# Kernel optimization log

Hardware: AMD Instinct MI355X
Metric: run time of the kernel (lower is better)

## Reference

```python
import jax, jax.numpy as jnp
import numpy as np

D_MODEL = 1024
N_HEAD = 16
AGENT_NUM = 256


def setup_inputs() -> dict:
    key = jax.random.key(0)
    ks = jax.random.split(key, 11)
    B, S, D = 4, 2048, D_MODEL
    s = 1.0 / np.sqrt(D)
    return {
        "q": jax.random.normal(ks[0], (B, S, D), jnp.float32),
        "k": jax.random.normal(ks[1], (B, S, D), jnp.float32),
        "v": jax.random.normal(ks[2], (B, S, D), jnp.float32),
        "Wq": jax.random.normal(ks[3], (D, D), jnp.float32) * s,
        "bq": jnp.zeros((D,), jnp.float32),
        "Wk": jax.random.normal(ks[4], (D, D), jnp.float32) * s,
        "bk": jnp.zeros((D,), jnp.float32),
        "Wv": jax.random.normal(ks[5], (D, D), jnp.float32) * s,
        "bv": jnp.zeros((D,), jnp.float32),
        "Wo": jax.random.normal(ks[6], (D, D), jnp.float32) * s,
        "bo": jnp.zeros((D,), jnp.float32),
    }


def _split_heads(x, n_head):
    B, S, D = x.shape
    return x.reshape(B, S, n_head, D // n_head).transpose(0, 2, 1, 3)  # [B,H,S,d]


def reference(q, k, v, Wq, bq, Wk, bk, Wv, bv, Wo, bo):
    B, S, D = q.shape
    H, A = N_HEAD, AGENT_NUM
    d = D // H
    scale = 1.0 / jnp.sqrt(jnp.asarray(d, q.dtype))

    # QKV linear projections (torch Linear: x @ W.T + b)
    qh = _split_heads(q @ Wq.T + bq, H)  # [B,H,S,d]
    kh = _split_heads(k @ Wk.T + bk, H)
    vh = _split_heads(v @ Wv.T + bv, H)

    # Agent tokens: average-pool queries along sequence down to A tokens
    agent = qh.reshape(B, H, A, S // A, d).mean(axis=3)  # [B,H,A,d]

    # Stage 1: agents aggregate from keys/values (softmax over S)
    agent_attn = jax.nn.softmax(
        jnp.einsum("bhad,bhsd->bhas", agent, kh) * scale, axis=-1)  # [B,H,A,S]
    agent_v = jnp.einsum("bhas,bhsd->bhad", agent_attn, vh)  # [B,H,A,d]

    # Stage 2: queries attend to agent tokens (softmax over A)
    q_attn = jax.nn.softmax(
        jnp.einsum("bhsd,bhad->bhsa", qh, agent) * scale, axis=-1)  # [B,H,S,A]
    out_h = jnp.einsum("bhsa,bhad->bhsd", q_attn, agent_v)  # [B,H,S,d]

    # concat heads + output projection
    out = out_h.transpose(0, 2, 1, 3).reshape(B, S, D)
    out = out @ Wo.T + bo
    return out, q_attn
```

## Files before the change

### kernel.cpp

```cpp
#include <hip/hip_runtime.h>

constexpr int Bsz = 4, Ssz = 2048, Dsz = 1024, Hn = 16, dh = 64, An = 256;

typedef __attribute__((ext_vector_type(8))) short bf16x8;
typedef __attribute__((ext_vector_type(4))) float f32x4;

__device__ __forceinline__ unsigned short f2bf_rn(float f) {
    unsigned int u = __float_as_uint(f);
    return (unsigned short)((u + 0x7FFFu + ((u >> 16) & 1u)) >> 16);
}
__device__ __forceinline__ float bf2f(unsigned short h) {
    return __uint_as_float(((unsigned int)h) << 16);
}
__device__ __forceinline__ void bf_split(float f, unsigned short& hi, unsigned short& lo) {
    hi = f2bf_rn(f);
    lo = f2bf_rn(f - bf2f(hi));
}
__device__ __forceinline__ void gload16(const unsigned short* g, unsigned short* l) {
    __builtin_amdgcn_global_load_lds(
        (const __attribute__((address_space(1))) unsigned int*)g,
        (__attribute__((address_space(3))) unsigned int*)l, 16, 0, 0);
}
__device__ __forceinline__ bf16x8 gfrag(const unsigned short* g) {
    return *reinterpret_cast<const bf16x8*>(g);
}
__device__ __forceinline__ void make8(float4 a, float4 b, bf16x8& hi8, bf16x8& lo8) {
    float v[8] = {a.x, a.y, a.z, a.w, b.x, b.y, b.z, b.w};
    #pragma unroll
    for (int i = 0; i < 8; ++i) {
        unsigned short h, l;
        bf_split(v[i], h, l);
        hi8[i] = (short)h; lo8[i] = (short)l;
    }
}


template<int LOGC, int NISS>
__device__ __forceinline__ void stage_tile(const unsigned short* __restrict__ g, long rowStride,
                                           unsigned short* lbase, int t) {
    const int wid = t >> 6;
    #pragma unroll
    for (int i = 0; i < NISS; ++i) {
        int slot = i * 256 + t;
        int r = slot >> LOGC;
        int c = slot & ((1 << LOGC) - 1);
        int cs = (c ^ (r & 7)) & ((1 << LOGC) - 1);
        gload16(g + (long)r * rowStride + cs * 8, lbase + (i * 256 + wid * 64) * 8);
    }
}
template<int ROWLEN>
__device__ __forceinline__ bf16x8 fragR(const unsigned short* buf, int row, int ks, int lane) {
    int c = ks * 4 + (lane >> 4);
    int cs = (c ^ (row & 7)) & (ROWLEN / 8 - 1);
    return *reinterpret_cast<const bf16x8*>(buf + row * ROWLEN + cs * 8);
}

__global__ __launch_bounds__(256)
void split_kernel(const float* __restrict__ x, unsigned short* __restrict__ hi,
                  unsigned short* __restrict__ lo, int n4)
{
    int i = blockIdx.x * 256 + threadIdx.x;
    if (i >= n4) return;
    float4 v = reinterpret_cast<const float4*>(x)[i];
    ushort4 h, l;
    bf_split(v.x, h.x, l.x);
    bf_split(v.y, h.y, l.y);
    bf_split(v.z, h.z, l.z);
    bf_split(v.w, h.w, l.w);
    reinterpret_cast<ushort4*>(hi)[i] = h;
    reinterpret_cast<ushort4*>(lo)[i] = l;
}

#define MT 128
#define BKm 32

__device__ __forceinline__ bf16x8 lds_frag(const unsigned short* buf, int baseRow, int lane) {
    int row = baseRow + (lane & 15);
    int c = lane >> 4;
    int idx = row * 32 + ((c ^ ((row >> 1) & 3)) << 3);
    return *reinterpret_cast<const bf16x8*>(buf + idx);
}

template<int OMODE>
__global__ __launch_bounds__(256, 2)
void gemm_nt_mfma3(const unsigned short* __restrict__ Ahi, const unsigned short* __restrict__ Alo,
                   const unsigned short* __restrict__ Bhi, const unsigned short* __restrict__ Blo,
                   const float* __restrict__ bias, float* __restrict__ Cf,
                   unsigned short* __restrict__ Chi, unsigned short* __restrict__ Clo,
                   int K, int N)
{
    __shared__ unsigned short lds[4 * 4096];
    const int t = threadIdx.x;
    const int lane = t & 63, wid = t >> 6;
    const int wr = wid >> 1, wc = wid & 1;
    const int m0 = blockIdx.y * MT, n0 = blockIdx.x * MT;

    const int srow0 = t >> 2;
    const int x4 = t & 3;
    const int ldsBase0 = (wid * 64) * 8;
    const int ldsBase1 = (256 + wid * 64) * 8;

    f32x4 acc[4][4];
    #pragma unroll
    for (int i = 0; i < 4; ++i)
        #pragma unroll
        for (int j = 0; j < 4; ++j)
            acc[i][j] = f32x4{0.f, 0.f, 0.f, 0.f};

    const unsigned short* gA[2] = {Ahi, Alo};
    const unsigned short* gB[2] = {Bhi, Blo};

    for (int k0 = 0; k0 < K; k0 += BKm) {
        #pragma unroll
        for (int hb = 0; hb < 2; ++hb) {
            {
                const unsigned short* G = gA[hb];
                int r0 = srow0, r1 = srow0 + 64;
                int c0 = x4 ^ ((r0 >> 1) & 3);
                int c1 = x4 ^ ((r1 >> 1) & 3);
                gload16(G + (size_t)(m0 + r0) * K + k0 + c0 * 8, lds + hb * 4096 + ldsBase0);
                gload16(G + (size_t)(m0 + r1) * K + k0 + c1 * 8, lds + hb * 4096 + ldsBase1);
            }
            {
                const unsigned short* G = gB[hb];
                int r0 = srow0, r1 = srow0 + 64;
                int c0 = x4 ^ ((r0 >> 1) & 3);
                int c1 = x4 ^ ((r1 >> 1) & 3);
                gload16(G + (size_t)(n0 + r0) * K + k0 + c0 * 8, lds + (2 + hb) * 4096 + ldsBase0);
                gload16(G + (size_t)(n0 + r1) * K + k0 + c1 * 8, lds + (2 + hb) * 4096 + ldsBase1);
            }
        }
        __syncthreads();

        bf16x8 ah[4], al[4], bh[4], bl[4];
        #pragma unroll
        for (int mi = 0; mi < 4; ++mi) {
            ah[mi] = lds_frag(lds + 0 * 4096, wr * 64 + mi * 16, lane);
            al[mi] = lds_frag(lds + 1 * 4096, wr * 64 + mi * 16, lane);
        }
        #pragma unroll
        for (int ni = 0; ni < 4; ++ni) {
            bh[ni] = lds_frag(lds + 2 * 4096, wc * 64 + ni * 16, lane);
            bl[ni] = lds_frag(lds + 3 * 4096, wc * 64 + ni * 16, lane);
        }
        #pragma unroll
        for (int mi = 0; mi < 4; ++mi)
            #pragma unroll
            for (int ni = 0; ni < 4; ++ni) {
                acc[mi][ni] = __builtin_amdgcn_mfma_f32_16x16x32_bf16(ah[mi], bh[ni], acc[mi][ni], 0, 0, 0);
                acc[mi][ni] = __builtin_amdgcn_mfma_f32_16x16x32_bf16(ah[mi], bl[ni], acc[mi][ni], 0, 0, 0);
                acc[mi][ni] = __builtin_amdgcn_mfma_f32_16x16x32_bf16(al[mi], bh[ni], acc[mi][ni], 0, 0, 0);
            }
        __syncthreads();
    }

    #pragma unroll
    for (int mi = 0; mi < 4; ++mi) {
        #pragma unroll
        for (int ni = 0; ni < 4; ++ni) {
            const int n = n0 + wc * 64 + ni * 16 + (lane & 15);
            const float bval = bias[n];
            #pragma unroll
            for (int j = 0; j < 4; ++j) {
                const int m = m0 + wr * 64 + mi * 16 + ((lane >> 4) << 2) + j;
                float val = acc[mi][ni][j] + bval;
                if constexpr (OMODE == 0) {
                    Cf[(size_t)m * N + n] = val;
                } else {
                    const int b = m >> 11, s = m & (Ssz - 1);
                    const int h = n >> 6, c = n & (dh - 1);
                    size_t idx;
                    if constexpr (OMODE == 1)
                        idx = (((size_t)(b * Hn + h)) * Ssz + s) * dh + c;
                    else if constexpr (OMODE == 2)
                        idx = (((size_t)(b * Hn + h)) * dh + c) * Ssz + s;
                    else
                        idx = (size_t)(b * Hn + h) * 131072
                            + (((s >> 4) * 2 + (c >> 5)) << 9)
                            + (((c >> 3) & 3) << 7) + ((s & 15) << 3) + (c & 7);
                    unsigned short hi, lo;
                    bf_split(val, hi, lo);
                    Chi[idx] = hi; Clo[idx] = lo;
                }
            }
        }
    }
}

__global__ __launch_bounds__(256)
void pool_agent(const unsigned short* __restrict__ qh_hi, const unsigned short* __restrict__ qh_lo,
                unsigned short* __restrict__ ag_hi, unsigned short* __restrict__ ag_lo)
{
    const int idx = blockIdx.x * 256 + threadIdx.x;
    const int c = idx & (dh - 1);
    const int a = (idx >> 6) & (An - 1);
    const int bh = idx >> 14;
    const size_t base = (size_t)bh * 131072
        + (((a >> 1) * 2 + (c >> 5)) << 9) + (((c >> 3) & 3) << 7)
        + ((8 * (a & 1)) << 3) + (c & 7);
    float s = 0.f;
    #pragma unroll
    for (int j = 0; j < 8; ++j)
        s += bf2f(qh_hi[base + j * 8]) + bf2f(qh_lo[base + j * 8]);
    s *= 0.125f;
    unsigned short hi, lo;
    bf_split(s, hi, lo);
    const size_t oidx = (size_t)bh * 16384
        + (((a >> 4) * 2 + (c >> 5)) << 9) + (((c >> 3) & 3) << 7)
        + ((a & 15) << 3) + (c & 7);
    ag_hi[oidx] = hi; ag_lo[oidx] = lo;
}

__global__ __launch_bounds__(256, 3)
void flash1(const unsigned short* __restrict__ ag_hi, const unsigned short* __restrict__ ag_lo,
            const unsigned short* __restrict__ kh_hi, const unsigned short* __restrict__ kh_lo,
            const unsigned short* __restrict__ vt_hi_g, const unsigned short* __restrict__ vt_lo_g,
            unsigned short* __restrict__ avt_hi, unsigned short* __restrict__ avt_lo)
{
    __shared__ unsigned short lds[24576];
    unsigned short* kth = lds;
    unsigned short* ktl = lds + 4096;
    unsigned short* vth = lds + 8192;
    unsigned short* vtl = lds + 12288;
    const int t = threadIdx.x;
    const int lane = t & 63, w = t >> 6;
    const int al15 = lane & 15, hi4 = lane >> 4;
    unsigned short* pwh = lds + 16384 + w * 2048;
    unsigned short* pwl = pwh + 1024;

    const int bh = blockIdx.y;
    const int a0 = blockIdx.x * 64;

    bf16x8 bqh[2], bql[2];
    {
        const size_t abase = (size_t)bh * 16384 + (size_t)((a0 >> 4) + w) * 1024;
        #pragma unroll
        for (int ks = 0; ks < 2; ++ks) {
            bqh[ks] = gfrag(ag_hi + abase + ks * 512 + lane * 8);
            bql[ks] = gfrag(ag_lo + abase + ks * 512 + lane * 8);
        }
    }

    f32x4 O[4];
    #pragma unroll
    for (int i = 0; i < 4; ++i) O[i] = f32x4{0.f, 0.f, 0.f, 0.f};
    float m_run = -INFINITY, l_run = 0.f;

    for (int s0 = 0; s0 < Ssz; s0 += 64) {
        stage_tile<3, 2>(kh_hi + ((size_t)bh * Ssz + s0) * dh, dh, kth, t);
        stage_tile<3, 2>(kh_lo + ((size_t)bh * Ssz + s0) * dh, dh, ktl, t);
        stage_tile<3, 2>(vt_hi_g + (size_t)bh * dh * Ssz + s0, Ssz, vth, t);
        stage_tile<3, 2>(vt_lo_g + (size_t)bh * dh * Ssz + s0, Ssz, vtl, t);
        __syncthreads();

        f32x4 sc[4];
        #pragma unroll
        for (int si = 0; si < 4; ++si) sc[si] = f32x4{0.f, 0.f, 0.f, 0.f};
        #pragma unroll
        for (int si = 0; si < 4; ++si)
            #pragma unroll
            for (int ks = 0; ks < 2; ++ks) {
                bf16x8 ah = fragR<64>(kth, si * 16 + al15, ks, lane);
                bf16x8 al = fragR<64>(ktl, si * 16 + al15, ks, lane);
                sc[si] = __builtin_amdgcn_mfma_f32_16x16x32_bf16(ah, bqh[ks], sc[si], 0, 0, 0);
                sc[si] = __builtin_amdgcn_mfma_f32_16x16x32_bf16(ah, bql[ks], sc[si], 0, 0, 0);
                sc[si] = __builtin_amdgcn_mfma_f32_16x16x32_bf16(al, bqh[ks], sc[si], 0, 0, 0);
            }

        float tmax = -INFINITY;
        #pragma unroll
        for (int si = 0; si < 4; ++si)
            #pragma unroll
            for (int j = 0; j < 4; ++j) {
                sc[si][j] *= 0.125f;
                tmax = fmaxf(tmax, sc[si][j]);
            }
        tmax = fmaxf(tmax, __shfl_xor(tmax, 16));
        tmax = fmaxf(tmax, __shfl_xor(tmax, 32));
        float newm = fmaxf(m_run, tmax);
        float fac = __expf(m_run - newm);
        float tsum = 0.f;
        #pragma unroll
        for (int si = 0; si < 4; ++si)
            #pragma unroll
            for (int j = 0; j < 4; ++j) {
                float p = __expf(sc[si][j] - newm);
                sc[si][j] = p;
                tsum += p;
            }
        tsum += __shfl_xor(tsum, 16);
        tsum += __shfl_xor(tsum, 32);
        l_run = l_run * fac + tsum;
        m_run = newm;

        #pragma unroll
        for (int si = 0; si < 4; ++si) {
            ushort4 h4, l4;
            bf_split(sc[si][0], h4.x, l4.x);
            bf_split(sc[si][1], h4.y, l4.y);
            bf_split(sc[si][2], h4.z, l4.z);
            bf_split(sc[si][3], h4.w, l4.w);
            int baseS = si * 16 + (hi4 << 2);
            int addr = al15 * 64 + (baseS ^ ((al15 & 7) << 3));
            *reinterpret_cast<ushort4*>(pwh + addr) = h4;
            *reinterpret_cast<ushort4*>(pwl + addr) = l4;
        }

        float fj[4];
        #pragma unroll
        for (int j = 0; j < 4; ++j) fj[j] = __shfl(fac, (hi4 << 2) + j);
        #pragma unroll
        for (int di = 0; di < 4; ++di)
            #pragma unroll
            for (int j = 0; j < 4; ++j) O[di][j] *= fj[j];

        #pragma unroll
        for (int ks = 0; ks < 2; ++ks) {
            bf16x8 pah = fragR<64>(pwh, al15, ks, lane);
            bf16x8 pal = fragR<64>(pwl, al15, ks, lane);
            #pragma unroll
            for (int di = 0; di < 4; ++di) {
                bf16x8 vh = fragR<64>(vth, di * 16 + al15, ks, lane);
                bf16x8 vl = fragR<64>(vtl, di * 16 + al15, ks, lane);
                O[di] = __builtin_amdgcn_mfma_f32_16x16x32_bf16(pah, vh, O[di], 0, 0, 0);
                O[di] = __builtin_amdgcn_mfma_f32_16x16x32_bf16(pah, vl, O[di], 0, 0, 0);
                O[di] = __builtin_amdgcn_mfma_f32_16x16x32_bf16(pal, vh, O[di], 0, 0, 0);
            }
        }
        __syncthreads();
    }

    float lj[4];
    #pragma unroll
    for (int j = 0; j < 4; ++j) lj[j] = __shfl(l_run, (hi4 << 2) + j);
    #pragma unroll
    for (int di = 0; di < 4; ++di) {
        ushort4 h4, l4;
        #pragma unroll
        for (int j = 0; j < 4; ++j) {
            float val = O[di][j] / lj[j];
            unsigned short hi, lo;
            bf_split(val, hi, lo);
            ((unsigned short*)&h4)[j] = hi;
            ((unsigned short*)&l4)[j] = lo;
        }
        const size_t oidx = (size_t)bh * 16384
            + (size_t)(di * 8 + (a0 >> 5) + (w >> 1)) * 512
            + (size_t)((2 * w + (hi4 >> 1)) & 3) * 128
            + al15 * 8 + (hi4 & 1) * 4;
        *reinterpret_cast<ushort4*>(avt_hi + oidx) = h4;
        *reinterpret_cast<ushort4*>(avt_lo + oidx) = l4;
    }
}

__global__ __launch_bounds__(256, 2)
void flash2(const unsigned short* __restrict__ qh_hi, const unsigned short* __restrict__ qh_lo,
            const unsigned short* __restrict__ ag_hi, const unsigned short* __restrict__ ag_lo,
            const unsigned short* __restrict__ avt_hi, const unsigned short* __restrict__ avt_lo,
            float* __restrict__ q_attn,
            unsigned short* __restrict__ xo_hi, unsigned short* __restrict__ xo_lo)
{
    __shared__ float plds[4][4096];

    const int t = threadIdx.x, lane = t & 63, w = t >> 6;
    const int al15 = lane & 15, hi4 = lane >> 4;
    const int bh = blockIdx.y;
    const int s0 = blockIdx.x * 64;
    float* P = plds[w];

    bf16x8 bqh[2], bql[2];
    {
        const size_t qbase = (size_t)bh * 131072 + (size_t)((s0 >> 4) + w) * 1024;
        #pragma unroll
        for (int ks = 0; ks < 2; ++ks) {
            bqh[ks] = gfrag(qh_hi + qbase + ks * 512 + lane * 8);
            bql[ks] = gfrag(qh_lo + qbase + ks * 512 + lane * 8);
        }
    }

    const unsigned short* agh = ag_hi + (size_t)bh * 16384;
    const unsigned short* agl = ag_lo + (size_t)bh * 16384;
    f32x4 acc[16];
    #pragma unroll
    for (int ai = 0; ai < 16; ++ai) acc[ai] = f32x4{0.f, 0.f, 0.f, 0.f};
    #pragma unroll
    for (int ai = 0; ai < 16; ++ai)
        #pragma unroll
        for (int ks = 0; ks < 2; ++ks) {
            bf16x8 ah = gfrag(agh + (ai * 2 + ks) * 512 + lane * 8);
            bf16x8 al = gfrag(agl + (ai * 2 + ks) * 512 + lane * 8);
            acc[ai] = __builtin_amdgcn_mfma_f32_16x16x32_bf16(ah, bqh[ks], acc[ai], 0, 0, 0);
            acc[ai] = __builtin_amdgcn_mfma_f32_16x16x32_bf16(ah, bql[ks], acc[ai], 0, 0, 0);
            acc[ai] = __builtin_amdgcn_mfma_f32_16x16x32_bf16(al, bqh[ks], acc[ai], 0, 0, 0);
        }

    float mx = -INFINITY;
    #pragma unroll
    for (int ai = 0; ai < 16; ++ai)
        #pragma unroll
        for (int j = 0; j < 4; ++j) {
            acc[ai][j] *= 0.125f;
            mx = fmaxf(mx, acc[ai][j]);
        }
    mx = fmaxf(mx, __shfl_xor(mx, 16));
    mx = fmaxf(mx, __shfl_xor(mx, 32));
    float sum = 0.f;
    #pragma unroll
    for (int ai = 0; ai < 16; ++ai)
        #pragma unroll
        for (int j = 0; j < 4; ++j) {
            float p = __expf(acc[ai][j] - mx);
            acc[ai][j] = p;
            sum += p;
        }
    sum += __shfl_xor(sum, 16);
    sum += __shfl_xor(sum, 32);
    const float inv = 1.0f / sum;

    #pragma unroll
    for (int ai = 0; ai < 16; ++ai) {
        float4 o;
        o.x = acc[ai][0] * inv; o.y = acc[ai][1] * inv;
        o.z = acc[ai][2] * inv; o.w = acc[ai][3] * inv;
        int pos4 = (ai * 4 + hi4) ^ (al15 & 7);
        *reinterpret_cast<float4*>(P + al15 * 256 + pos4 * 4) = o;
    }

    {
        float* qbase = q_attn + ((size_t)bh * Ssz + s0 + w * 16) * An;
        #pragma unroll
        for (int r = 0; r < 16; ++r) {
            float4 f = *reinterpret_cast<const float4*>(P + r * 256 + ((lane ^ (r & 7)) * 4));
            *reinterpret_cast<float4*>(qbase + r * An + lane * 4) = f;
        }
    }

    const unsigned short* avh_b = avt_hi + (size_t)bh * 16384;
    const unsigned short* avl_b = avt_lo + (size_t)bh * 16384;
    f32x4 O[4];
    #pragma unroll
    for (int i = 0; i < 4; ++i) O[i] = f32x4{0.f, 0.f, 0.f, 0.f};
    #pragma unroll
    for (int ks = 0; ks < 8; ++ks) {
        int p4 = ks * 8 + hi4 * 2;
        float4 fa = *reinterpret_cast<const float4*>(P + al15 * 256 + ((p4 ^ (al15 & 7)) * 4));
        float4 fb = *reinterpret_cast<const float4*>(P + al15 * 256 + (((p4 + 1) ^ (al15 & 7)) * 4));
        bf16x8 pah, pal;
        make8(fa, fb, pah, pal);
        #pragma unroll
        for (int di = 0; di < 4; ++di) {
            bf16x8 avh = gfrag(avh_b + (di * 8 + ks) * 512 + lane * 8);
            bf16x8 avl = gfrag(avl_b + (di * 8 + ks) * 512 + lane * 8);
            O[di] = __builtin_amdgcn_mfma_f32_16x16x32_bf16(pah, avh, O[di], 0, 0, 0);
            O[di] = __builtin_amdgcn_mfma_f32_16x16x32_bf16(pah, avl, O[di], 0, 0, 0);
            O[di] = __builtin_amdgcn_mfma_f32_16x16x32_bf16(pal, avh, O[di], 0, 0, 0);
        }
    }

    const int b = bh >> 4, h = bh & (Hn - 1);
    #pragma unroll
    for (int di = 0; di < 4; ++di)
        #pragma unroll
        for (int j = 0; j < 4; ++j) {
            float val = O[di][j];
            int sG = s0 + w * 16 + (hi4 << 2) + j;
            int dfull = h * dh + di * 16 + al15;
            size_t idx = ((size_t)b * Ssz + sG) * Dsz + dfull;
            unsigned short hi, lo;
            bf_split(val, hi, lo);
            xo_hi[idx] = hi; xo_lo[idx] = lo;
        }
}

extern "C" void kernel_launch(void* const* d_in, const int* in_sizes, int n_in,
                              void* d_out, int out_size, void* d_ws, size_t ws_size,
                              hipStream_t stream)
{
    const float* q  = (const float*)d_in[0];
    const float* k  = (const float*)d_in[1];
    const float* v  = (const float*)d_in[2];
    const float* Wq = (const float*)d_in[3];
    const float* bq = (const float*)d_in[4];
    const float* Wk = (const float*)d_in[5];
    const float* bk = (const float*)d_in[6];
    const float* Wv = (const float*)d_in[7];
    const float* bv = (const float*)d_in[8];
    const float* Wo = (const float*)d_in[9];
    const float* bo = (const float*)d_in[10];

    constexpr size_t BSD = (size_t)Bsz * Ssz * Dsz;
    constexpr size_t DD  = (size_t)Dsz * Dsz;
    constexpr size_t AGD = (size_t)Bsz * Hn * An * dh;

    float* out    = (float*)d_out;
    float* q_attn = out + BSD;

    unsigned short* u = (unsigned short*)d_ws;
    unsigned short* x_hi   = u;
    unsigned short* x_lo   = x_hi + BSD;
    unsigned short* qh_hi  = x_lo + BSD;
    unsigned short* qh_lo  = qh_hi + BSD;
    unsigned short* kh_hi  = qh_lo + BSD;
    unsigned short* kh_lo  = kh_hi + BSD;
    unsigned short* vt_hi  = kh_lo + BSD;
    unsigned short* vt_lo  = vt_hi + BSD;
    unsigned short* w_hi   = vt_lo + BSD;
    unsigned short* w_lo   = w_hi + DD;
    unsigned short* ag_hi  = w_lo + DD;
    unsigned short* ag_lo  = ag_hi + AGD;
    unsigned short* avt_hi = ag_lo + AGD;
    unsigned short* avt_lo = avt_hi + AGD;

    const int M = Bsz * Ssz;
    dim3 gmfma(Dsz / MT, M / MT, 1);

    split_kernel<<<BSD / 1024, 256, 0, stream>>>(q, x_hi, x_lo, BSD / 4);
    split_kernel<<<DD / 1024, 256, 0, stream>>>(Wq, w_hi, w_lo, DD / 4);
    gemm_nt_mfma3<3><<<gmfma, 256, 0, stream>>>(x_hi, x_lo, w_hi, w_lo, bq, nullptr, qh_hi, qh_lo, Dsz, Dsz);
    split_kernel<<<BSD / 1024, 256, 0, stream>>>(k, x_hi, x_lo, BSD / 4);
    split_kernel<<<DD / 1024, 256, 0, stream>>>(Wk, w_hi, w_lo, DD / 4);
    gemm_nt_mfma3<1><<<gmfma, 256, 0, stream>>>(x_hi, x_lo, w_hi, w_lo, bk, nullptr, kh_hi, kh_lo, Dsz, Dsz);
    split_kernel<<<BSD / 1024, 256, 0, stream>>>(v, x_hi, x_lo, BSD / 4);
    split_kernel<<<DD / 1024, 256, 0, stream>>>(Wv, w_hi, w_lo, DD / 4);
    gemm_nt_mfma3<2><<<gmfma, 256, 0, stream>>>(x_hi, x_lo, w_hi, w_lo, bv, nullptr, vt_hi, vt_lo, Dsz, Dsz);

    pool_agent<<<AGD / 256, 256, 0, stream>>>(qh_hi, qh_lo, ag_hi, ag_lo);

    flash1<<<dim3(An / 64, Bsz * Hn), 256, 0, stream>>>(
        ag_hi, ag_lo, kh_hi, kh_lo, vt_hi, vt_lo, avt_hi, avt_lo);

    flash2<<<dim3(Ssz / 64, Bsz * Hn), 256, 0, stream>>>(
        qh_hi, qh_lo, ag_hi, ag_lo, avt_hi, avt_lo, q_attn, x_hi, x_lo);

    split_kernel<<<DD / 1024, 256, 0, stream>>>(Wo, w_hi, w_lo, DD / 4);
    gemm_nt_mfma3<0><<<gmfma, 256, 0, stream>>>(x_hi, x_lo, w_hi, w_lo, bo, out, nullptr, nullptr, Dsz, Dsz);
}
```

Measured before the change: 416.3 us.

## Batch QKV splits and GEMMs into single launches, remap flash grids

Merges the three input split launches and four weight split launches into two batched kernels, and fuses the three QKV projection GEMMs into one launch using blockIdx.z to pick operands and output layout. The flash kernels switch to a 1D grid with head index in the low bits, so consecutive blocks cover different heads. This removes several kernel launches and lets the QKV GEMMs fill the GPU at once, at the cost of a larger workspace for separate split buffers and runtime branching on z in the epilogue.

Result: slower. 434.3 us (+4.3%).

```diff
diff --git a/kernel.cpp b/kernel.cpp
--- a/kernel.cpp
+++ b/kernel.cpp
@@ -1,6 +1,9 @@
 #include <hip/hip_runtime.h>
 
 constexpr int Bsz = 4, Ssz = 2048, Dsz = 1024, Hn = 16, dh = 64, An = 256;
+constexpr size_t BSD = (size_t)Bsz * Ssz * Dsz;
+constexpr size_t DD  = (size_t)Dsz * Dsz;
+constexpr size_t AGD = (size_t)Bsz * Hn * An * dh;
 
 typedef __attribute__((ext_vector_type(8))) short bf16x8;
 typedef __attribute__((ext_vector_type(4))) float f32x4;
@@ -33,7 +36,6 @@
         hi8[i] = (short)h; lo8[i] = (short)l;
     }
 }
-
 
 template<int LOGC, int NISS>
 __device__ __forceinline__ void stage_tile(const unsigned short* __restrict__ g, long rowStride,
@@ -55,13 +57,10 @@
     return *reinterpret_cast<const bf16x8*>(buf + row * ROWLEN + cs * 8);
 }
 
-__global__ __launch_bounds__(256)
-void split_kernel(const float* __restrict__ x, unsigned short* __restrict__ hi,
-                  unsigned short* __restrict__ lo, int n4)
-{
-    int i = blockIdx.x * 256 + threadIdx.x;
-    if (i >= n4) return;
-    float4 v = reinterpret_cast<const float4*>(x)[i];
+__device__ __forceinline__ void split4(const float* __restrict__ src,
+                                       unsigned short* __restrict__ hi,
+                                       unsigned short* __restrict__ lo, int i) {
+    float4 v = reinterpret_cast<const float4*>(src)[i];
     ushort4 h, l;
     bf_split(v.x, h.x, l.x);
     bf_split(v.y, h.y, l.y);
@@ -71,6 +70,32 @@
     reinterpret_cast<ushort4*>(lo)[i] = l;
 }
 
+__global__ __launch_bounds__(256)
+void split_inputs(const float* __restrict__ q, const float* __restrict__ k,
+                  const float* __restrict__ v,
+                  unsigned short* __restrict__ xq_hi, unsigned short* __restrict__ xq_lo,
+                  unsigned short* __restrict__ xk_hi, unsigned short* __restrict__ xk_lo,
+                  unsigned short* __restrict__ xv_hi, unsigned short* __restrict__ xv_lo)
+{
+    const int job = blockIdx.y;
+    const float* src = (job == 0) ? q : (job == 1) ? k : v;
+    unsigned short* dh_ = (job == 0) ? xq_hi : (job == 1) ? xk_hi : xv_hi;
+    unsigned short* dl_ = (job == 0) ? xq_lo : (job == 1) ? xk_lo : xv_lo;
+    int i = blockIdx.x * 256 + threadIdx.x;
+    split4(src, dh_, dl_, i);
+}
+
+__global__ __launch_bounds__(256)
+void split_weights(const float* __restrict__ Wq, const float* __restrict__ Wk,
+                   const float* __restrict__ Wv, const float* __restrict__ Wo,
+                   unsigned short* __restrict__ w_hi, unsigned short* __restrict__ w_lo)
+{
+    const int job = blockIdx.y;
+    const float* src = (job == 0) ? Wq : (job == 1) ? Wk : (job == 2) ? Wv : Wo;
+    int i = blockIdx.x * 256 + threadIdx.x;
+    split4(src, w_hi + job * DD, w_lo + job * DD, i);
+}
+
 #define MT 128
 #define BKm 32
 
@@ -81,78 +106,87 @@
     return *reinterpret_cast<const bf16x8*>(buf + idx);
 }
 
-template<int OMODE>
+#define GEMM_BODY(Ahi, Alo, Bhi, Blo)                                                   \
+    __shared__ unsigned short lds[4 * 4096];                                            \
+    const int t = threadIdx.x;                                                          \
+    const int lane = t & 63, wid = t >> 6;                                              \
+    const int wr = wid >> 1, wc = wid & 1;                                              \
+    const int m0 = blockIdx.y * MT, n0 = blockIdx.x * MT;                               \
+    const int srow0 = t >> 2;                                                           \
+    const int x4 = t & 3;                                                               \
+    const int ldsBase0 = (wid * 64) * 8;                                                \
+    const int ldsBase1 = (256 + wid * 64) * 8;                                          \
+    f32x4 acc[4][4];                                                                    \
+    _Pragma("unroll")                                                                   \
+    for (int i = 0; i < 4; ++i)                                                         \
+        _Pragma("unroll")                                                               \
+        for (int j = 0; j < 4; ++j)                                                     \
+            acc[i][j] = f32x4{0.f, 0.f, 0.f, 0.f};                                      \
+    const unsigned short* gA[2] = {Ahi, Alo};                                           \
+    const unsigned short* gB[2] = {Bhi, Blo};                                           \
+    for (int k0 = 0; k0 < Dsz; k0 += BKm) {                                             \
+        _Pragma("unroll")                                                               \
+        for (int hb = 0; hb < 2; ++hb) {                                                \
+            {                                                                           \
+                const unsigned short* G = gA[hb];                                       \
+                int r0 = srow0, r1 = srow0 + 64;                                        \
+                int c0 = x4 ^ ((r0 >> 1) & 3);                                          \
+                int c1 = x4 ^ ((r1 >> 1) & 3);                                          \
+                gload16(G + (size_t)(m0 + r0) * Dsz + k0 + c0 * 8, lds + hb * 4096 + ldsBase0); \
+                gload16(G + (size_t)(m0 + r1) * Dsz + k0 + c1 * 8, lds + hb * 4096 + ldsBase1); \
+            }                                                                           \
+            {                                                                           \
+                const unsigned short* G = gB[hb];                                       \
+                int r0 = srow0, r1 = srow0 + 64;                                        \
+                int c0 = x4 ^ ((r0 >> 1) & 3);                                          \
+                int c1 = x4 ^ ((r1 >> 1) & 3);                                          \
+                gload16(G + (size_t)(n0 + r0) * Dsz + k0 + c0 * 8, lds + (2 + hb) * 4096 + ldsBase0); \
+                gload16(G + (size_t)(n0 + r1) * Dsz + k0 + c1 * 8, lds + (2 + hb) * 4096 + ldsBase1); \
+            }                                                                           \
+        }                                                                               \
+        __syncthreads();                                                                \
+        bf16x8 ah[4], al[4], bh[4], bl[4];                                              \
+        _Pragma("unroll")                                                               \
+        for (int mi = 0; mi < 4; ++mi) {                                                \
+            ah[mi] = lds_frag(lds + 0 * 4096, wr * 64 + mi * 16, lane);                 \
+            al[mi] = lds_frag(lds + 1 * 4096, wr * 64 + mi * 16, lane);                 \
+        }                                                                               \
+        _Pragma("unroll")                                                               \
+        for (int ni = 0; ni < 4; ++ni) {                                                \
+            bh[ni] = lds_frag(lds + 2 * 4096, wc * 64 + ni * 16, lane);                 \
+            bl[ni] = lds_frag(lds + 3 * 4096, wc * 64 + ni * 16, lane);                 \
+        }                                                                               \
+        _Pragma("unroll")                                                               \
+        for (int mi = 0; mi < 4; ++mi)                                                  \
+            _Pragma("unroll")                                                           \
+            for (int ni = 0; ni < 4; ++ni) {                                            \
+                acc[mi][ni] = __builtin_amdgcn_mfma_f32_16x16x32_bf16(ah[mi], bh[ni], acc[mi][ni], 0, 0, 0); \
+                acc[mi][ni] = __builtin_amdgcn_mfma_f32_16x16x32_bf16(ah[mi], bl[ni], acc[mi][ni], 0, 0, 0); \
+                acc[mi][ni] = __builtin_amdgcn_mfma_f32_16x16x32_bf16(al[mi], bh[ni], acc[mi][ni], 0, 0, 0); \
+            }                                                                           \
+        __syncthreads();                                                                \
+    }
+
 __global__ __launch_bounds__(256, 2)
-void gemm_nt_mfma3(const unsigned short* __restrict__ Ahi, const unsigned short* __restrict__ Alo,
-                   const unsigned short* __restrict__ Bhi, const unsigned short* __restrict__ Blo,
-                   const float* __restrict__ bias, float* __restrict__ Cf,
-                   unsigned short* __restrict__ Chi, unsigned short* __restrict__ Clo,
-                   int K, int N)
-{
-    __shared__ unsigned short lds[4 * 4096];
-    const int t = threadIdx.x;
-    const int lane = t & 63, wid = t >> 6;
-    const int wr = wid >> 1, wc = wid & 1;
-    const int m0 = blockIdx.y * MT, n0 = blockIdx.x * MT;
-
-    const int srow0 = t >> 2;
-    const int x4 = t & 3;
-    const int ldsBase0 = (wid * 64) * 8;
-    const int ldsBase1 = (256 + wid * 64) * 8;
-
-    f32x4 acc[4][4];
-    #pragma unroll
-    for (int i = 0; i < 4; ++i)
-        #pragma unroll
-        for (int j = 0; j < 4; ++j)
-            acc[i][j] = f32x4{0.f, 0.f, 0.f, 0.f};
-
-    const unsigned short* gA[2] = {Ahi, Alo};
-    const unsigned short* gB[2] = {Bhi, Blo};
-
-    for (int k0 = 0; k0 < K; k0 += BKm) {
-        #pragma unroll
-        for (int hb = 0; hb < 2; ++hb) {
-            {
-                const unsigned short* G = gA[hb];
-                int r0 = srow0, r1 = srow0 + 64;
-                int c0 = x4 ^ ((r0 >> 1) & 3);
-                int c1 = x4 ^ ((r1 >> 1) & 3);
-                gload16(G + (size_t)(m0 + r0) * K + k0 + c0 * 8, lds + hb * 4096 + ldsBase0);
-                gload16(G + (size_t)(m0 + r1) * K + k0 + c1 * 8, lds + hb * 4096 + ldsBase1);
-            }
-            {
-                const unsigned short* G = gB[hb];
-                int r0 = srow0, r1 = srow0 + 64;
-                int c0 = x4 ^ ((r0 >> 1) & 3);
-                int c1 = x4 ^ ((r1 >> 1) & 3);
-                gload16(G + (size_t)(n0 + r0) * K + k0 + c0 * 8, lds + (2 + hb) * 4096 + ldsBase0);
-                gload16(G + (size_t)(n0 + r1) * K + k0 + c1 * 8, lds + (2 + hb) * 4096 + ldsBase1);
-            }
-        }
-        __syncthreads();
-
-        bf16x8 ah[4], al[4], bh[4], bl[4];
-        #pragma unroll
-        for (int mi = 0; mi < 4; ++mi) {
-            ah[mi] = lds_frag(lds + 0 * 4096, wr * 64 + mi * 16, lane);
-            al[mi] = lds_frag(lds + 1 * 4096, wr * 64 + mi * 16, lane);
-        }
-        #pragma unroll
-        for (int ni = 0; ni < 4; ++ni) {
-            bh[ni] = lds_frag(lds + 2 * 4096, wc * 64 + ni * 16, lane);
-            bl[ni] = lds_frag(lds + 3 * 4096, wc * 64 + ni * 16, lane);
-        }
-        #pragma unroll
-        for (int mi = 0; mi < 4; ++mi)
-            #pragma unroll
-            for (int ni = 0; ni < 4; ++ni) {
-                acc[mi][ni] = __builtin_amdgcn_mfma_f32_16x16x32_bf16(ah[mi], bh[ni], acc[mi][ni], 0, 0, 0);
-                acc[mi][ni] = __builtin_amdgcn_mfma_f32_16x16x32_bf16(ah[mi], bl[ni], acc[mi][ni], 0, 0, 0);
-                acc[mi][ni] = __builtin_amdgcn_mfma_f32_16x16x32_bf16(al[mi], bh[ni], acc[mi][ni], 0, 0, 0);
-            }
-        __syncthreads();
-    }
+void gemm_qkv(const unsigned short* __restrict__ xq_hi, const unsigned short* __restrict__ xq_lo,
+              const unsigned short* __restrict__ xk_hi, const unsigned short* __restrict__ xk_lo,
+              const unsigned short* __restrict__ xv_hi, const unsigned short* __restrict__ xv_lo,
+              const unsigned short* __restrict__ w_hi, const unsigned short* __restrict__ w_lo,
+              const float* __restrict__ bq, const float* __restrict__ bk, const float* __restrict__ bv,
+              unsigned short* __restrict__ qh_hi, unsigned short* __restrict__ qh_lo,
+              unsigned short* __restrict__ kh_hi, unsigned short* __restrict__ kh_lo,
+              unsigned short* __restrict__ vt_hi, unsigned short* __restrict__ vt_lo)
+{
+    const int z = blockIdx.z;
+    const unsigned short* Ahi = (z == 0) ? xq_hi : (z == 1) ? xk_hi : xv_hi;
+    const unsigned short* Alo = (z == 0) ? xq_lo : (z == 1) ? xk_lo : xv_lo;
+    const unsigned short* Bhi = w_hi + (size_t)z * DD;
+    const unsigned short* Blo = w_lo + (size_t)z * DD;
+    const float* bias = (z == 0) ? bq : (z == 1) ? bk : bv;
+    unsigned short* Chi = (z == 0) ? qh_hi : (z == 1) ? kh_hi : vt_hi;
+    unsigned short* Clo = (z == 0) ? qh_lo : (z == 1) ? kh_lo : vt_lo;
+
+    GEMM_BODY(Ahi, Alo, Bhi, Blo)
 
     #pragma unroll
     for (int mi = 0; mi < 4; ++mi) {
@@ -164,24 +198,42 @@
             for (int j = 0; j < 4; ++j) {
                 const int m = m0 + wr * 64 + mi * 16 + ((lane >> 4) << 2) + j;
                 float val = acc[mi][ni][j] + bval;
-                if constexpr (OMODE == 0) {
-                    Cf[(size_t)m * N + n] = val;
-                } else {
-                    const int b = m >> 11, s = m & (Ssz - 1);
-                    const int h = n >> 6, c = n & (dh - 1);
-                    size_t idx;
-                    if constexpr (OMODE == 1)
-                        idx = (((size_t)(b * Hn + h)) * Ssz + s) * dh + c;
-                    else if constexpr (OMODE == 2)
-                        idx = (((size_t)(b * Hn + h)) * dh + c) * Ssz + s;
-                    else
-                        idx = (size_t)(b * Hn + h) * 131072
-                            + (((s >> 4) * 2 + (c >> 5)) << 9)
-                            + (((c >> 3) & 3) << 7) + ((s & 15) << 3) + (c & 7);
-                    unsigned short hi, lo;
-                    bf_split(val, hi, lo);
-                    Chi[idx] = hi; Clo[idx] = lo;
-                }
+                const int b = m >> 11, s = m & (Ssz - 1);
+                const int h = n >> 6, c = n & (dh - 1);
+                size_t idx;
+                if (z == 0)
+                    idx = (size_t)(b * Hn + h) * 131072
+                        + (((s >> 4) * 2 + (c >> 5)) << 9)
+                        + (((c >> 3) & 3) << 7) + ((s & 15) << 3) + (c & 7);
+                else if (z == 1)
+                    idx = (((size_t)(b * Hn + h)) * Ssz + s) * dh + c;
+                else
+                    idx = (((size_t)(b * Hn + h)) * dh + c) * Ssz + s;
+                unsigned short hi, lo;
+                bf_split(val, hi, lo);
+                Chi[idx] = hi; Clo[idx] = lo;
+            }
+        }
+    }
+}
+
+__global__ __launch_bounds__(256, 2)
+void gemm_out(const unsigned short* __restrict__ Ahi_, const unsigned short* __restrict__ Alo_,
+              const unsigned short* __restrict__ Bhi_, const unsigned short* __restrict__ Blo_,
+              const float* __restrict__ bias, float* __restrict__ Cf)
+{
+    GEMM_BODY(Ahi_, Alo_, Bhi_, Blo_)
+
+    #pragma unroll
+    for (int mi = 0; mi < 4; ++mi) {
+        #pragma unroll
+        for (int ni = 0; ni < 4; ++ni) {
+            const int n = n0 + wc * 64 + ni * 16 + (lane & 15);
+            const float bval = bias[n];
+            #pragma unroll
+            for (int j = 0; j < 4; ++j) {
+                const int m = m0 + wr * 64 + mi * 16 + ((lane >> 4) << 2) + j;
+                Cf[(size_t)m * Dsz + n] = acc[mi][ni][j] + bval;
             }
         }
     }
@@ -228,8 +280,8 @@
     unsigned short* pwh = lds + 16384 + w * 2048;
     unsigned short* pwl = pwh + 1024;
 
-    const int bh = blockIdx.y;
-    const int a0 = blockIdx.x * 64;
+    const int bh = blockIdx.x & 63;
+    const int a0 = (blockIdx.x >> 6) * 64;
 
     bf16x8 bqh[2], bql[2];
     {
@@ -364,8 +416,8 @@
 
     const int t = threadIdx.x, lane = t & 63, w = t >> 6;
     const int al15 = lane & 15, hi4 = lane >> 4;
-    const int bh = blockIdx.y;
-    const int s0 = blockIdx.x * 64;
+    const int bh = blockIdx.x & 63;
+    const int s0 = (blockIdx.x >> 6) * 64;
     float* P = plds[w];
 
     bf16x8 bqh[2], bql[2];
@@ -488,25 +540,25 @@
     const float* Wo = (const float*)d_in[9];
     const float* bo = (const float*)d_in[10];
 
-    constexpr size_t BSD = (size_t)Bsz * Ssz * Dsz;
-    constexpr size_t DD  = (size_t)Dsz * Dsz;
-    constexpr size_t AGD = (size_t)Bsz * Hn * An * dh;
-
     float* out    = (float*)d_out;
     float* q_attn = out + BSD;
 
     unsigned short* u = (unsigned short*)d_ws;
-    unsigned short* x_hi   = u;
-    unsigned short* x_lo   = x_hi + BSD;
-    unsigned short* qh_hi  = x_lo + BSD;
+    unsigned short* xq_hi  = u;
+    unsigned short* xq_lo  = xq_hi + BSD;
+    unsigned short* xk_hi  = xq_lo + BSD;
+    unsigned short* xk_lo  = xk_hi + BSD;
+    unsigned short* xv_hi  = xk_lo + BSD;
+    unsigned short* xv_lo  = xv_hi + BSD;
+    unsigned short* qh_hi  = xv_lo + BSD;
     unsigned short* qh_lo  = qh_hi + BSD;
     unsigned short* kh_hi  = qh_lo + BSD;
     unsigned short* kh_lo  = kh_hi + BSD;
     unsigned short* vt_hi  = kh_lo + BSD;
     unsigned short* vt_lo  = vt_hi + BSD;
     unsigned short* w_hi   = vt_lo + BSD;
-    unsigned short* w_lo   = w_hi + DD;
-    unsigned short* ag_hi  = w_lo + DD;
+    unsigned short* w_lo   = w_hi + 4 * DD;
+    unsigned short* ag_hi  = w_lo + 4 * DD;
     unsigned short* ag_lo  = ag_hi + AGD;
     unsigned short* avt_hi = ag_lo + AGD;
     unsigned short* avt_lo = avt_hi + AGD;
@@ -514,24 +566,23 @@
     const int M = Bsz * Ssz;
     dim3 gmfma(Dsz / MT, M / MT, 1);
 
-    split_kernel<<<BSD / 1024, 256, 0, stream>>>(q, x_hi, x_lo, BSD / 4);
-    split_kernel<<<DD / 1024, 256, 0, stream>>>(Wq, w_hi, w_lo, DD / 4);
-    gemm_nt_mfma3<3><<<gmfma, 256, 0, stream>>>(x_hi, x_lo, w_hi, w_lo, bq, nullptr, qh_hi, qh_lo, Dsz, Dsz);
-    split_kernel<<<BSD / 1024, 256, 0, stream>>>(k, x_hi, x_lo, BSD / 4);
-    split_kernel<<<DD / 1024, 256, 0, stream>>>(Wk, w_hi, w_lo, DD / 4);
-    gemm_nt_mfma3<1><<<gmfma, 256, 0, stream>>>(x_hi, x_lo, w_hi, w_lo, bk, nullptr, kh_hi, kh_lo, Dsz, Dsz);
-    split_kernel<<<BSD / 1024, 256, 0, stream>>>(v, x_hi, x_lo, BSD / 4);
-    split_kernel<<<DD / 1024, 256, 0, stream>>>(Wv, w_hi, w_lo, DD / 4);
-    gemm_nt_mfma3<2><<<gmfma, 256, 0, stream>>>(x_hi, x_lo, w_hi, w_lo, bv, nullptr, vt_hi, vt_lo, Dsz, Dsz);
+    split_inputs<<<dim3(BSD / 1024, 3), 256, 0, stream>>>(
+        q, k, v, xq_hi, xq_lo, xk_hi, xk_lo, xv_hi, xv_lo);
+    split_weights<<<dim3(DD / 1024, 4), 256, 0, stream>>>(
+        Wq, Wk, Wv, Wo, w_hi, w_lo);
+
+    gemm_qkv<<<dim3(Dsz / MT, M / MT, 3), 256, 0, stream>>>(
+        xq_hi, xq_lo, xk_hi, xk_lo, xv_hi, xv_lo, w_hi, w_lo,
+        bq, bk, bv, qh_hi, qh_lo, kh_hi, kh_lo, vt_hi, vt_lo);
 
     pool_agent<<<AGD / 256, 256, 0, stream>>>(qh_hi, qh_lo, ag_hi, ag_lo);
 
-    flash1<<<dim3(An / 64, Bsz * Hn), 256, 0, stream>>>(
+    flash1<<<256, 256, 0, stream>>>(
         ag_hi, ag_lo, kh_hi, kh_lo, vt_hi, vt_lo, avt_hi, avt_lo);
 
-    flash2<<<dim3(Ssz / 64, Bsz * Hn), 256, 0, stream>>>(
-        qh_hi, qh_lo, ag_hi, ag_lo, avt_hi, avt_lo, q_attn, x_hi, x_lo);
-
-    split_kernel<<<DD / 1024, 256, 0, stream>>>(Wo, w_hi, w_lo, DD / 4);
-    gemm_nt_mfma3<0><<<gmfma, 256, 0, stream>>>(x_hi, x_lo, w_hi, w_lo, bo, out, nullptr, nullptr, Dsz, Dsz);
-}
+    flash2<<<2048, 256, 0, stream>>>(
+        qh_hi, qh_lo, ag_hi, ag_lo, avt_hi, avt_lo, q_attn, xq_hi, xq_lo);
+
+    gemm_out<<<gmfma, 256, 0, stream>>>(
+        xq_hi, xq_lo, w_hi + 3 * DD, w_lo + 3 * DD, bo, out);
+}
```
